# Kernel tuning notes

Measured on AMD Instinct MI355X. Metric: run time of the kernel, lower is better.

Reference implementation:

```python
import jax, jax.numpy as jnp
import numpy as np
import math

B, S, D_MODEL = 4, 2048, 1024
H, D_QK, D_V = 16, 64, 64


def setup_inputs() -> dict:
    key = jax.random.key(0)
    ks = jax.random.split(key, 12)
    s = 0.02
    return {
        "input_q": jax.random.normal(ks[0], (B, S, D_MODEL), jnp.float32),
        "input_k": jax.random.normal(ks[1], (B, S, D_MODEL), jnp.float32),
        "input_v": jax.random.normal(ks[2], (B, S, D_MODEL), jnp.float32),
        # per-head projection weights stacked over heads: [H, out, d_model] (torch Linear layout)
        "WQw": jax.random.normal(ks[3], (H, D_QK, D_MODEL), jnp.float32) * s,
        "WQb": jax.random.normal(ks[4], (H, D_QK), jnp.float32) * s,
        "WKw": jax.random.normal(ks[5], (H, D_QK, D_MODEL), jnp.float32) * s,
        "WKb": jax.random.normal(ks[6], (H, D_QK), jnp.float32) * s,
        "WVw": jax.random.normal(ks[7], (H, D_V, D_MODEL), jnp.float32) * s,
        "WVb": jax.random.normal(ks[8], (H, D_V), jnp.float32) * s,
        # output projection: Linear(H*D_V, D_MODEL)
        "Ww": jax.random.normal(ks[9], (D_MODEL, H * D_V), jnp.float32) * s,
        "Wb": jax.random.normal(ks[10], (D_MODEL,), jnp.float32) * s,
    }


def _mha(input_q, input_k, input_v, WQw, WQb, WKw, WKb, WVw, WVb, Ww, Wb):
    # per-head projections: [B,H,S,d]
    Q = jnp.einsum("bsd,hed->bhse", input_q, WQw) + WQb[None, :, None, :]
    K = jnp.einsum("bsd,hed->bhse", input_k, WKw) + WKb[None, :, None, :]
    V = jnp.einsum("bsd,hvd->bhsv", input_v, WVw) + WVb[None, :, None, :]
    scores = jnp.einsum("bhse,bhte->bhst", Q, K)  # [B,H,S,S]
    # causal mask added BEFORE division by sqrt(d_model), as in original
    causal = jnp.triu(jnp.full((S, S), -jnp.inf, scores.dtype), k=1)
    scores = (scores + causal) / math.sqrt(D_MODEL)  # NOTE: d_model, not d_qk
    attn = jax.nn.softmax(scores, axis=-1)
    ctx = jnp.einsum("bhst,bhtv->bhsv", attn, V)  # [B,H,S,D_V]
    concat = ctx.transpose(0, 2, 1, 3).reshape(B, S, H * D_V)  # head-order concat
    return concat @ Ww.T + Wb


def reference(input_q, input_k, input_v, WQw, WQb, WKw, WKb, WVw, WVb, Ww, Wb):
    return _mha(input_q, input_k, input_v, WQw, WQb, WKw, WKb, WVw, WVb, Ww, Wb)
```

## Files before the change

### kernel.cpp

```cpp
#include <hip/hip_runtime.h>
#include <hip/hip_bf16.h>

typedef __attribute__((ext_vector_type(8))) short bf16x8;
typedef __attribute__((ext_vector_type(4))) short bf16x4;
typedef __attribute__((ext_vector_type(4))) float f32x4;
typedef __attribute__((ext_vector_type(16))) float f32x16;

#define MFMA16(a, b, c) __builtin_amdgcn_mfma_f32_16x16x32_bf16(a, b, c, 0, 0, 0)
#define MFMA32(a, b, c) __builtin_amdgcn_mfma_f32_32x32x16_bf16(a, b, c, 0, 0, 0)

__device__ __forceinline__ unsigned short f2bfn(float f) {
#if defined(__gfx950__)
  __bf16 h = (__bf16)f;
  return __builtin_bit_cast(unsigned short, h);
#else
  union { float f; unsigned u; } x; x.f = f;
  unsigned r = x.u + 0x7fffu + ((x.u >> 16) & 1u);
  return (unsigned short)(r >> 16);
#endif
}

__device__ __forceinline__ void plswap(unsigned& a, unsigned& b) {
  auto r = __builtin_amdgcn_permlane32_swap(a, b, false, false);
  a = r[0];
  b = r[1];
}

__device__ __forceinline__ unsigned cvtpk(float lo, float hi) {
  unsigned w;
  asm("v_cvt_pk_bf16_f32 %0, %1, %2" : "=v"(w) : "v"(lo), "v"(hi));
  return w;
}

__device__ __forceinline__ void cvt_body(const float* __restrict__ s,
                                         unsigned short* __restrict__ d, int n8) {
  int i = blockIdx.x * blockDim.x + threadIdx.x;
  int st = gridDim.x * blockDim.x;
  for (; i < n8; i += st) {
    const float4* sp = reinterpret_cast<const float4*>(s) + 2 * (size_t)i;
    float4 a = sp[0], b = sp[1];
    bf16x8 o;
    o[0] = (short)f2bfn(a.x); o[1] = (short)f2bfn(a.y);
    o[2] = (short)f2bfn(a.z); o[3] = (short)f2bfn(a.w);
    o[4] = (short)f2bfn(b.x); o[5] = (short)f2bfn(b.y);
    o[6] = (short)f2bfn(b.z); o[7] = (short)f2bfn(b.w);
    reinterpret_cast<bf16x8*>(d)[i] = o;
  }
}

__global__ void cvt1_kernel(const float* __restrict__ s, unsigned short* __restrict__ d, int n8) {
  cvt_body(s, d, n8);
}

__global__ void cvt_w_kernel(const float* s0, const float* s1, const float* s2, const float* s3,
                             unsigned short* d0, unsigned short* d1, unsigned short* d2,
                             unsigned short* d3, int n8) {
  const float* s; unsigned short* d;
  switch (blockIdx.y) {
    case 0: s = s0; d = d0; break;
    case 1: s = s1; d = d1; break;
    case 2: s = s2; d = d2; break;
    default: s = s3; d = d3; break;
  }
  cvt_body(s, d, n8);
}

template <int MODE>
__global__ __launch_bounds__(256) void gemm_kernel(
    const unsigned short* __restrict__ Av, const unsigned short* __restrict__ Bv,
    const float* __restrict__ bias, void* __restrict__ outv,
    int M, int N, int K) {
  constexpr int BM = 128, BN = 128, BK = 64;
  __shared__ __align__(16) unsigned short As[2][BM * BK];
  __shared__ __align__(16) unsigned short Bs[2][BN * BK];
  const int tid = threadIdx.x;
  const int lane = tid & 63, wave = tid >> 6;
  const int wr = wave >> 1, wc = wave & 1;
  const int m0 = blockIdx.y * BM, n0 = blockIdx.x * BN;
  const int rb = lane & 15, g = lane >> 4;
  const int swz = ((lane & 7) ^ ((lane >> 3) & 7)) * 8;
  f32x4 acc[4][4] = {};

  const unsigned short* Ab = Av + (size_t)m0 * K;
  const unsigned short* Bb = Bv + (size_t)n0 * K;

  auto stage = [&](int buf, int k0) {
#pragma unroll
    for (int i = 0; i < 4; ++i) {
      const int c = wave * 256 + i * 64 + lane;
      const int r = c >> 3;
      __builtin_amdgcn_global_load_lds(
          (const __attribute__((address_space(1))) unsigned int*)(Ab + (size_t)r * K + k0 + swz),
          (__attribute__((address_space(3))) unsigned int*)&As[buf][c * 8], 16, 0, 0);
      __builtin_amdgcn_global_load_lds(
          (const __attribute__((address_space(1))) unsigned int*)(Bb + (size_t)r * K + k0 + swz),
          (__attribute__((address_space(3))) unsigned int*)&Bs[buf][c * 8], 16, 0, 0);
    }
  };

  const int nt = K / BK;
  stage(0, 0);
  int cur = 0;
  for (int t = 0; t < nt; ++t) {
    __syncthreads();
    if (t + 1 < nt) stage(cur ^ 1, (t + 1) * BK);
    const unsigned short* A_ = As[cur];
    const unsigned short* B_ = Bs[cur];
#pragma unroll
    for (int kc = 0; kc < 2; ++kc) {
      bf16x8 af[4], bfr[4];
#pragma unroll
      for (int mi = 0; mi < 4; ++mi)
        af[mi] = *reinterpret_cast<const bf16x8*>(
            &A_[(wr * 64 + mi * 16 + rb) * 64 + (((kc * 4 + g) ^ (rb & 7)) * 8)]);
#pragma unroll
      for (int ni = 0; ni < 4; ++ni)
        bfr[ni] = *reinterpret_cast<const bf16x8*>(
            &B_[(wc * 64 + ni * 16 + rb) * 64 + (((kc * 4 + g) ^ (rb & 7)) * 8)]);
#pragma unroll
      for (int mi = 0; mi < 4; ++mi)
#pragma unroll
        for (int ni = 0; ni < 4; ++ni)
          acc[mi][ni] = MFMA16(af[mi], bfr[ni], acc[mi][ni]);
    }
    cur ^= 1;
  }

#pragma unroll
  for (int mi = 0; mi < 4; ++mi) {
#pragma unroll
    for (int ni = 0; ni < 4; ++ni) {
      int col = n0 + wc * 64 + ni * 16 + rb;
      if constexpr (MODE != 2) {
        float bv = bias[col];
#pragma unroll
        for (int j = 0; j < 4; ++j) {
          int row = m0 + wr * 64 + mi * 16 + g * 4 + j;
          float v = acc[mi][ni][j] + bv;
          if constexpr (MODE == 0) {
            int b = row >> 11, s = row & 2047;
            int h = col >> 6, e = col & 63;
            ((unsigned short*)outv)[((size_t)(b * 16 + h) * 2048 + s) * 64 + e] = f2bfn(v);
          } else {
            ((float*)outv)[(size_t)row * N + col] = v;
          }
        }
      } else {
        int bb = col >> 11, s = col & 2047;
#pragma unroll
        for (int j = 0; j < 4; ++j) {
          int row = m0 + wr * 64 + mi * 16 + g * 4 + j;
          float v = acc[mi][ni][j] + bias[row];
          int h = row >> 6, e = row & 63;
          ((unsigned short*)outv)[((size_t)(bb * 16 + h) * 64 + e) * 2048 + s] = f2bfn(v);
        }
      }
    }
  }
}

__global__ __launch_bounds__(256) void attn3_kernel(
    const unsigned short* __restrict__ Qp, const unsigned short* __restrict__ Kp,
    const unsigned short* __restrict__ Vtp, unsigned short* __restrict__ ctx) {
  constexpr int S = 2048;
  __shared__ __align__(16) unsigned short Ks[2][64 * 64];
  __shared__ __align__(16) unsigned short Vs[2][64 * 64];
  const int bx = blockIdx.x;
  const int bh = bx & 63;
  const int qti = 15 - (bx >> 6);
  const int q0 = qti * 128;
  const int tid = threadIdx.x, wave = tid >> 6, lane = tid & 63;
  const int l31 = lane & 31, hb = lane >> 5, hb4 = hb * 4;
  const int x7 = l31 & 7;
  const int qw = q0 + wave * 32;
  const unsigned short* Qb = Qp + (size_t)bh * S * 64;
  const unsigned short* Kb = Kp + (size_t)bh * S * 64;
  const unsigned short* Vb = Vtp + (size_t)bh * 64 * S;

  bf16x8 qg[4];
#pragma unroll
  for (int kc = 0; kc < 4; ++kc)
    qg[kc] = *reinterpret_cast<const bf16x8*>(
        Qb + (size_t)(qw + l31) * 64 + 16 * kc + 8 * hb);

  float m2 = -1e30f, nm2 = 0.f, lsum = 0.f;
  f32x16 o[2] = {};
  const float sc = 0.03125f * 1.4426950408889634f;
  const float TH = 8.0f / sc;
  const int sswz = ((lane & 7) ^ (lane >> 3)) * 8;
  const int nt = qti * 2 + 2;

  auto stage = [&](int buf, int kv0) {
#pragma unroll
    for (int i = 0; i < 2; ++i) {
      const int ci = (wave * 2 + i) * 64 + lane;
      const int r = (wave * 2 + i) * 8 + (lane >> 3);
      __builtin_amdgcn_global_load_lds(
          (const __attribute__((address_space(1))) unsigned int*)(Kb + (size_t)(kv0 + r) * 64 + sswz),
          (__attribute__((address_space(3))) unsigned int*)&Ks[buf][ci * 8], 16, 0, 0);
      __builtin_amdgcn_global_load_lds(
          (const __attribute__((address_space(1))) unsigned int*)(Vb + (size_t)r * S + kv0 + sswz),
          (__attribute__((address_space(3))) unsigned int*)&Vs[buf][ci * 8], 16, 0, 0);
    }
  };

  stage(0, 0);

  for (int it = 0; it < nt; ++it) {
    __syncthreads();
    if (it + 1 < nt) stage((it + 1) & 1, 64 * (it + 1));
    const int kv0 = 64 * it;
    if (kv0 <= qw + 31) {
      const unsigned short* K_ = Ks[it & 1];
      const unsigned short* V_ = Vs[it & 1];
      f32x16 sacc[2] = {};
      __builtin_amdgcn_s_setprio(1);
#pragma unroll
      for (int kc = 0; kc < 4; ++kc) {
        bf16x8 kf0 = *reinterpret_cast<const bf16x8*>(
            &K_[l31 * 64 + ((2 * kc + hb) ^ x7) * 8]);
        bf16x8 kf1 = *reinterpret_cast<const bf16x8*>(
            &K_[(32 + l31) * 64 + ((2 * kc + hb) ^ x7) * 8]);
        sacc[0] = MFMA32(kf0, qg[kc], sacc[0]);
        sacc[1] = MFMA32(kf1, qg[kc], sacc[1]);
      }
      __builtin_amdgcn_s_setprio(0);
      if (kv0 + 63 > qw) {
        const int qrel = qw + l31 - kv0;
#pragma unroll
        for (int mi = 0; mi < 2; ++mi)
#pragma unroll
          for (int r = 0; r < 16; ++r) {
            int koff = 32 * mi + (r & 3) + 8 * (r >> 2) + hb4;
            if (koff > qrel) sacc[mi][r] = -1e30f;
          }
      }
      float mt = -1e30f;
#pragma unroll
      for (int mi = 0; mi < 2; ++mi)
#pragma unroll
        for (int r = 0; r < 16; ++r) mt = fmaxf(mt, sacc[mi][r]);
      mt = fmaxf(mt, __shfl_xor(mt, 32, 64));
      if (__any((int)(mt > m2 + TH))) {
        float mn = fmaxf(m2, mt);
        float corr = __builtin_amdgcn_exp2f((m2 - mn) * sc);
        m2 = mn; nm2 = -mn * sc;
        lsum *= corr;
#pragma unroll
        for (int db = 0; db < 2; ++db)
#pragma unroll
          for (int r = 0; r < 16; ++r) o[db][r] *= corr;
      }
      float rs = 0.f;
      unsigned pw[2][8];
#pragma unroll
      for (int mi = 0; mi < 2; ++mi) {
        float p[16];
#pragma unroll
        for (int r = 0; r < 16; ++r) {
          p[r] = __builtin_amdgcn_exp2f(fmaf(sacc[mi][r], sc, nm2));
          rs += p[r];
        }
#pragma unroll
        for (int i = 0; i < 8; ++i) pw[mi][i] = cvtpk(p[2 * i], p[2 * i + 1]);
      }
      lsum += rs;
#pragma unroll
      for (int mi = 0; mi < 2; ++mi) {
        plswap(pw[mi][0], pw[mi][2]);
        plswap(pw[mi][1], pw[mi][3]);
        plswap(pw[mi][4], pw[mi][6]);
        plswap(pw[mi][5], pw[mi][7]);
      }
      __builtin_amdgcn_s_setprio(1);
#pragma unroll
      for (int c = 0; c < 4; ++c) {
        union { unsigned u[4]; bf16x8 v; } pu;
        pu.u[0] = pw[c >> 1][(c & 1) * 4 + 0];
        pu.u[1] = pw[c >> 1][(c & 1) * 4 + 1];
        pu.u[2] = pw[c >> 1][(c & 1) * 4 + 2];
        pu.u[3] = pw[c >> 1][(c & 1) * 4 + 3];
#pragma unroll
        for (int db = 0; db < 2; ++db) {
          bf16x8 vf = *reinterpret_cast<const bf16x8*>(
              &V_[(32 * db + l31) * 64 + ((2 * c + hb) ^ x7) * 8]);
          o[db] = MFMA32(vf, pu.v, o[db]);
        }
      }
      __builtin_amdgcn_s_setprio(0);
    }
  }

  const float tot = lsum + __shfl_xor(lsum, 32, 64);
  const float inv = 1.0f / tot;
  const int b = bh >> 4, h = bh & 15;
  const int q = qw + l31;
  unsigned short* cp = ctx + ((size_t)(b * 2048 + q) * 1024) + h * 64;
#pragma unroll
  for (int db = 0; db < 2; ++db)
#pragma unroll
    for (int i = 0; i < 8; ++i) {
      unsigned w = cvtpk(o[db][2 * i] * inv, o[db][2 * i + 1] * inv);
      int d = 32 * db + ((2 * i) & 3) + 8 * (i >> 1) + hb4;
      *reinterpret_cast<unsigned*>(cp + d) = w;
    }
}

extern "C" void kernel_launch(void* const* d_in, const int* in_sizes, int n_in,
                              void* d_out, int out_size, void* d_ws, size_t ws_size,
                              hipStream_t stream) {
  const float* in_q = (const float*)d_in[0];
  const float* in_k = (const float*)d_in[1];
  const float* in_v = (const float*)d_in[2];
  const float* WQw = (const float*)d_in[3];
  const float* WQb = (const float*)d_in[4];
  const float* WKw = (const float*)d_in[5];
  const float* WKb = (const float*)d_in[6];
  const float* WVw = (const float*)d_in[7];
  const float* WVb = (const float*)d_in[8];
  const float* Ww  = (const float*)d_in[9];
  const float* Wb  = (const float*)d_in[10];
  float* out = (float*)d_out;

  constexpr size_t PROJ = (size_t)4 * 16 * 2048 * 64;
  constexpr size_t WSZ = (size_t)1024 * 1024;
  unsigned short* wsp = (unsigned short*)d_ws;
  unsigned short* Qp   = wsp;
  unsigned short* Kp   = wsp + PROJ;
  unsigned short* Vt   = wsp + 2 * PROJ;
  unsigned short* in16 = wsp + 3 * PROJ;
  unsigned short* ctx  = in16;
  unsigned short* wq16 = wsp + 4 * PROJ;
  unsigned short* wk16 = wq16 + WSZ;
  unsigned short* wv16 = wk16 + WSZ;
  unsigned short* ww16 = wv16 + WSZ;

  cvt_w_kernel<<<dim3(256, 4), 256, 0, stream>>>(WQw, WKw, WVw, Ww,
                                                 wq16, wk16, wv16, ww16, (int)(WSZ / 8));
  cvt1_kernel<<<2048, 256, 0, stream>>>(in_q, in16, (int)(PROJ / 8));
  gemm_kernel<0><<<dim3(8, 64), 256, 0, stream>>>(in16, wq16, WQb, Qp, 8192, 1024, 1024);
  cvt1_kernel<<<2048, 256, 0, stream>>>(in_k, in16, (int)(PROJ / 8));
  gemm_kernel<0><<<dim3(8, 64), 256, 0, stream>>>(in16, wk16, WKb, Kp, 8192, 1024, 1024);
  cvt1_kernel<<<2048, 256, 0, stream>>>(in_v, in16, (int)(PROJ / 8));
  gemm_kernel<2><<<dim3(64, 8), 256, 0, stream>>>(wv16, in16, WVb, Vt, 1024, 8192, 1024);

  attn3_kernel<<<1024, 256, 0, stream>>>(Qp, Kp, Vt, ctx);

  gemm_kernel<1><<<dim3(8, 64), 256, 0, stream>>>(ctx, ww16, Wb, out, 8192, 1024, 1024);
}
```

Measured before the change: 192.5 us.

## Pair causal query tiles per block and deepen K/V staging to four buffers

The attention kernel now launches half as many blocks, and each block handles two query tiles (qti and 15-qti), so every block does a similar amount of causal work. K/V staging moves from double to quad buffering, with explicit vmcnt waits and raw s_barrier so three tiles of loads stay in flight. The softmax max and sum reductions become tree reductions, and the fp32-to-bf16 conversion uses packed cvt instructions. In exchange, LDS use doubles to 64KB per block, which may reduce occupancy, and the grid of 512 blocks may underfill the GPU.

After: 194.2 us. About the same (+0.9%).

```diff
diff --git a/kernel.cpp b/kernel.cpp
--- a/kernel.cpp
+++ b/kernel.cpp
@@ -5,6 +5,7 @@
 typedef __attribute__((ext_vector_type(4))) short bf16x4;
 typedef __attribute__((ext_vector_type(4))) float f32x4;
 typedef __attribute__((ext_vector_type(16))) float f32x16;
+typedef __attribute__((ext_vector_type(4))) unsigned uint4v;
 
 #define MFMA16(a, b, c) __builtin_amdgcn_mfma_f32_16x16x32_bf16(a, b, c, 0, 0, 0)
 #define MFMA32(a, b, c) __builtin_amdgcn_mfma_f32_32x32x16_bf16(a, b, c, 0, 0, 0)
@@ -39,12 +40,10 @@
   for (; i < n8; i += st) {
     const float4* sp = reinterpret_cast<const float4*>(s) + 2 * (size_t)i;
     float4 a = sp[0], b = sp[1];
-    bf16x8 o;
-    o[0] = (short)f2bfn(a.x); o[1] = (short)f2bfn(a.y);
-    o[2] = (short)f2bfn(a.z); o[3] = (short)f2bfn(a.w);
-    o[4] = (short)f2bfn(b.x); o[5] = (short)f2bfn(b.y);
-    o[6] = (short)f2bfn(b.z); o[7] = (short)f2bfn(b.w);
-    reinterpret_cast<bf16x8*>(d)[i] = o;
+    uint4v o;
+    o[0] = cvtpk(a.x, a.y); o[1] = cvtpk(a.z, a.w);
+    o[2] = cvtpk(b.x, b.y); o[3] = cvtpk(b.z, b.w);
+    reinterpret_cast<uint4v*>(d)[i] = o;
   }
 }
 
@@ -159,36 +158,24 @@
   }
 }
 
-__global__ __launch_bounds__(256) void attn3_kernel(
+__global__ __launch_bounds__(256) void attn4_kernel(
     const unsigned short* __restrict__ Qp, const unsigned short* __restrict__ Kp,
     const unsigned short* __restrict__ Vtp, unsigned short* __restrict__ ctx) {
   constexpr int S = 2048;
-  __shared__ __align__(16) unsigned short Ks[2][64 * 64];
-  __shared__ __align__(16) unsigned short Vs[2][64 * 64];
+  __shared__ __align__(16) unsigned short Ks[4][64 * 64];
+  __shared__ __align__(16) unsigned short Vs[4][64 * 64];
   const int bx = blockIdx.x;
   const int bh = bx & 63;
-  const int qti = 15 - (bx >> 6);
-  const int q0 = qti * 128;
+  const int pi = bx >> 6;
   const int tid = threadIdx.x, wave = tid >> 6, lane = tid & 63;
   const int l31 = lane & 31, hb = lane >> 5, hb4 = hb * 4;
   const int x7 = l31 & 7;
-  const int qw = q0 + wave * 32;
   const unsigned short* Qb = Qp + (size_t)bh * S * 64;
   const unsigned short* Kb = Kp + (size_t)bh * S * 64;
   const unsigned short* Vb = Vtp + (size_t)bh * 64 * S;
-
-  bf16x8 qg[4];
-#pragma unroll
-  for (int kc = 0; kc < 4; ++kc)
-    qg[kc] = *reinterpret_cast<const bf16x8*>(
-        Qb + (size_t)(qw + l31) * 64 + 16 * kc + 8 * hb);
-
-  float m2 = -1e30f, nm2 = 0.f, lsum = 0.f;
-  f32x16 o[2] = {};
   const float sc = 0.03125f * 1.4426950408889634f;
   const float TH = 8.0f / sc;
   const int sswz = ((lane & 7) ^ (lane >> 3)) * 8;
-  const int nt = qti * 2 + 2;
 
   auto stage = [&](int buf, int kv0) {
 #pragma unroll
@@ -204,106 +191,137 @@
     }
   };
 
-  stage(0, 0);
-
-  for (int it = 0; it < nt; ++it) {
-    __syncthreads();
-    if (it + 1 < nt) stage((it + 1) & 1, 64 * (it + 1));
-    const int kv0 = 64 * it;
-    if (kv0 <= qw + 31) {
-      const unsigned short* K_ = Ks[it & 1];
-      const unsigned short* V_ = Vs[it & 1];
-      f32x16 sacc[2] = {};
-      __builtin_amdgcn_s_setprio(1);
-#pragma unroll
-      for (int kc = 0; kc < 4; ++kc) {
-        bf16x8 kf0 = *reinterpret_cast<const bf16x8*>(
-            &K_[l31 * 64 + ((2 * kc + hb) ^ x7) * 8]);
-        bf16x8 kf1 = *reinterpret_cast<const bf16x8*>(
-            &K_[(32 + l31) * 64 + ((2 * kc + hb) ^ x7) * 8]);
-        sacc[0] = MFMA32(kf0, qg[kc], sacc[0]);
-        sacc[1] = MFMA32(kf1, qg[kc], sacc[1]);
+  for (int half = 0; half < 2; ++half) {
+    const int qti = half ? pi : 15 - pi;
+    const int qw = qti * 128 + wave * 32;
+
+    bf16x8 qg[4];
+#pragma unroll
+    for (int kc = 0; kc < 4; ++kc)
+      qg[kc] = *reinterpret_cast<const bf16x8*>(
+          Qb + (size_t)(qw + l31) * 64 + 16 * kc + 8 * hb);
+
+    float m2 = -1e30f, nm2 = 0.f, lsum = 0.f;
+    f32x16 o[2] = {};
+    const int nt = qti * 2 + 2;
+
+    if (half) __syncthreads();
+    stage(0, 0);
+    stage(1, 64);
+    stage(2, 128);
+
+    for (int it = 0; it < nt; ++it) {
+      const int rem = nt - 1 - it;
+      if (rem >= 2)      asm volatile("s_waitcnt vmcnt(8)" ::: "memory");
+      else if (rem == 1) asm volatile("s_waitcnt vmcnt(4)" ::: "memory");
+      else               asm volatile("s_waitcnt vmcnt(0)" ::: "memory");
+      __builtin_amdgcn_s_barrier();
+      __builtin_amdgcn_sched_barrier(0);
+      if (it + 3 < nt) stage((it + 3) & 3, 64 * (it + 3));
+      const int kv0 = 64 * it;
+      if (kv0 <= qw + 31) {
+        const unsigned short* K_ = Ks[it & 3];
+        const unsigned short* V_ = Vs[it & 3];
+        f32x16 sacc[2] = {};
+        __builtin_amdgcn_s_setprio(1);
+#pragma unroll
+        for (int kc = 0; kc < 4; ++kc) {
+          bf16x8 kf0 = *reinterpret_cast<const bf16x8*>(
+              &K_[l31 * 64 + ((2 * kc + hb) ^ x7) * 8]);
+          bf16x8 kf1 = *reinterpret_cast<const bf16x8*>(
+              &K_[(32 + l31) * 64 + ((2 * kc + hb) ^ x7) * 8]);
+          sacc[0] = MFMA32(kf0, qg[kc], sacc[0]);
+          sacc[1] = MFMA32(kf1, qg[kc], sacc[1]);
+        }
+        __builtin_amdgcn_s_setprio(0);
+        if (kv0 + 63 > qw) {
+          const int qrel = qw + l31 - kv0;
+#pragma unroll
+          for (int mi = 0; mi < 2; ++mi)
+#pragma unroll
+            for (int r = 0; r < 16; ++r) {
+              int koff = 32 * mi + (r & 3) + 8 * (r >> 2) + hb4;
+              if (koff > qrel) sacc[mi][r] = -1e30f;
+            }
+        }
+        float mx[16];
+#pragma unroll
+        for (int r = 0; r < 16; ++r) mx[r] = fmaxf(sacc[0][r], sacc[1][r]);
+#pragma unroll
+        for (int s = 8; s > 0; s >>= 1)
+#pragma unroll
+          for (int r = 0; r < s; ++r) mx[r] = fmaxf(mx[r], mx[r + s]);
+        float mt = fmaxf(mx[0], __shfl_xor(mx[0], 32, 64));
+        if (__any((int)(mt > m2 + TH))) {
+          float mn = fmaxf(m2, mt);
+          float corr = __builtin_amdgcn_exp2f((m2 - mn) * sc);
+          m2 = mn; nm2 = -mn * sc;
+          lsum *= corr;
+#pragma unroll
+          for (int db = 0; db < 2; ++db)
+#pragma unroll
+            for (int r = 0; r < 16; ++r) o[db][r] *= corr;
+        }
+        float p0[16], p1[16];
+#pragma unroll
+        for (int r = 0; r < 16; ++r)
+          p0[r] = __builtin_amdgcn_exp2f(fmaf(sacc[0][r], sc, nm2));
+#pragma unroll
+        for (int r = 0; r < 16; ++r)
+          p1[r] = __builtin_amdgcn_exp2f(fmaf(sacc[1][r], sc, nm2));
+        unsigned pw[2][8];
+#pragma unroll
+        for (int i = 0; i < 8; ++i) pw[0][i] = cvtpk(p0[2 * i], p0[2 * i + 1]);
+#pragma unroll
+        for (int i = 0; i < 8; ++i) pw[1][i] = cvtpk(p1[2 * i], p1[2 * i + 1]);
+        float a[16];
+#pragma unroll
+        for (int r = 0; r < 16; ++r) a[r] = p0[r] + p1[r];
+#pragma unroll
+        for (int s = 8; s > 0; s >>= 1)
+#pragma unroll
+          for (int r = 0; r < s; ++r) a[r] += a[r + s];
+        lsum += a[0];
+#pragma unroll
+        for (int mi = 0; mi < 2; ++mi) {
+          plswap(pw[mi][0], pw[mi][2]);
+          plswap(pw[mi][1], pw[mi][3]);
+          plswap(pw[mi][4], pw[mi][6]);
+          plswap(pw[mi][5], pw[mi][7]);
+        }
+        __builtin_amdgcn_s_setprio(1);
+#pragma unroll
+        for (int c = 0; c < 4; ++c) {
+          union { unsigned u[4]; bf16x8 v; } pu;
+          pu.u[0] = pw[c >> 1][(c & 1) * 4 + 0];
+          pu.u[1] = pw[c >> 1][(c & 1) * 4 + 1];
+          pu.u[2] = pw[c >> 1][(c & 1) * 4 + 2];
+          pu.u[3] = pw[c >> 1][(c & 1) * 4 + 3];
+#pragma unroll
+          for (int db = 0; db < 2; ++db) {
+            bf16x8 vf = *reinterpret_cast<const bf16x8*>(
+                &V_[(32 * db + l31) * 64 + ((2 * c + hb) ^ x7) * 8]);
+            o[db] = MFMA32(vf, pu.v, o[db]);
+          }
+        }
+        __builtin_amdgcn_s_setprio(0);
       }
-      __builtin_amdgcn_s_setprio(0);
-      if (kv0 + 63 > qw) {
-        const int qrel = qw + l31 - kv0;
-#pragma unroll
-        for (int mi = 0; mi < 2; ++mi)
-#pragma unroll
-          for (int r = 0; r < 16; ++r) {
-            int koff = 32 * mi + (r & 3) + 8 * (r >> 2) + hb4;
-            if (koff > qrel) sacc[mi][r] = -1e30f;
-          }
+    }
+
+    const float tot = lsum + __shfl_xor(lsum, 32, 64);
+    const float inv = 1.0f / tot;
+    const int b = bh >> 4, h = bh & 15;
+    const int q = qw + l31;
+    unsigned short* cp = ctx + ((size_t)(b * 2048 + q) * 1024) + h * 64;
+#pragma unroll
+    for (int db = 0; db < 2; ++db)
+#pragma unroll
+      for (int i = 0; i < 8; ++i) {
+        unsigned w = cvtpk(o[db][2 * i] * inv, o[db][2 * i + 1] * inv);
+        int d = 32 * db + ((2 * i) & 3) + 8 * (i >> 1) + hb4;
+        *reinterpret_cast<unsigned*>(cp + d) = w;
       }
-      float mt = -1e30f;
-#pragma unroll
-      for (int mi = 0; mi < 2; ++mi)
-#pragma unroll
-        for (int r = 0; r < 16; ++r) mt = fmaxf(mt, sacc[mi][r]);
-      mt = fmaxf(mt, __shfl_xor(mt, 32, 64));
-      if (__any((int)(mt > m2 + TH))) {
-        float mn = fmaxf(m2, mt);
-        float corr = __builtin_amdgcn_exp2f((m2 - mn) * sc);
-        m2 = mn; nm2 = -mn * sc;
-        lsum *= corr;
-#pragma unroll
-        for (int db = 0; db < 2; ++db)
-#pragma unroll
-          for (int r = 0; r < 16; ++r) o[db][r] *= corr;
-      }
-      float rs = 0.f;
-      unsigned pw[2][8];
-#pragma unroll
-      for (int mi = 0; mi < 2; ++mi) {
-        float p[16];
-#pragma unroll
-        for (int r = 0; r < 16; ++r) {
-          p[r] = __builtin_amdgcn_exp2f(fmaf(sacc[mi][r], sc, nm2));
-          rs += p[r];
-        }
-#pragma unroll
-        for (int i = 0; i < 8; ++i) pw[mi][i] = cvtpk(p[2 * i], p[2 * i + 1]);
-      }
-      lsum += rs;
-#pragma unroll
-      for (int mi = 0; mi < 2; ++mi) {
-        plswap(pw[mi][0], pw[mi][2]);
-        plswap(pw[mi][1], pw[mi][3]);
-        plswap(pw[mi][4], pw[mi][6]);
-        plswap(pw[mi][5], pw[mi][7]);
-      }
-      __builtin_amdgcn_s_setprio(1);
-#pragma unroll
-      for (int c = 0; c < 4; ++c) {
-        union { unsigned u[4]; bf16x8 v; } pu;
-        pu.u[0] = pw[c >> 1][(c & 1) * 4 + 0];
-        pu.u[1] = pw[c >> 1][(c & 1) * 4 + 1];
-        pu.u[2] = pw[c >> 1][(c & 1) * 4 + 2];
-        pu.u[3] = pw[c >> 1][(c & 1) * 4 + 3];
-#pragma unroll
-        for (int db = 0; db < 2; ++db) {
-          bf16x8 vf = *reinterpret_cast<const bf16x8*>(
-              &V_[(32 * db + l31) * 64 + ((2 * c + hb) ^ x7) * 8]);
-          o[db] = MFMA32(vf, pu.v, o[db]);
-        }
-      }
-      __builtin_amdgcn_s_setprio(0);
-    }
-  }
-
-  const float tot = lsum + __shfl_xor(lsum, 32, 64);
-  const float inv = 1.0f / tot;
-  const int b = bh >> 4, h = bh & 15;
-  const int q = qw + l31;
-  unsigned short* cp = ctx + ((size_t)(b * 2048 + q) * 1024) + h * 64;
-#pragma unroll
-  for (int db = 0; db < 2; ++db)
-#pragma unroll
-    for (int i = 0; i < 8; ++i) {
-      unsigned w = cvtpk(o[db][2 * i] * inv, o[db][2 * i + 1] * inv);
-      int d = 32 * db + ((2 * i) & 3) + 8 * (i >> 1) + hb4;
-      *reinterpret_cast<unsigned*>(cp + d) = w;
-    }
+  }
 }
 
 extern "C" void kernel_launch(void* const* d_in, const int* in_sizes, int n_in,
@@ -344,7 +362,7 @@
   cvt1_kernel<<<2048, 256, 0, stream>>>(in_v, in16, (int)(PROJ / 8));
   gemm_kernel<2><<<dim3(64, 8), 256, 0, stream>>>(wv16, in16, WVb, Vt, 1024, 8192, 1024);
 
-  attn3_kernel<<<1024, 256, 0, stream>>>(Qp, Kp, Vt, ctx);
+  attn4_kernel<<<512, 256, 0, stream>>>(Qp, Kp, Vt, ctx);
 
   gemm_kernel<1><<<dim3(8, 64), 256, 0, stream>>>(ctx, ww16, Wb, out, 8192, 1024, 1024);
 }
```
